# Kernel tuning notes

Hardware: AMD Instinct MI355X
Metric: run time of the kernel (lower is better)

Reference implementation:

```python
import jax, jax.numpy as jnp
import numpy as np


def setup_inputs() -> dict:
    key = jax.random.key(0)
    k1, k2, k3 = jax.random.split(key, 3)
    N, F, E, H = 50000, 256, 800000, 4
    P = F // H + 1            # proj = 65
    dk = P * H                # 260
    x = jax.random.normal(k1, (N, F), dtype=jnp.float32)
    W = jax.random.normal(k2, (2 * dk, F), dtype=jnp.float32) * 0.02
    b = jnp.zeros((2 * dk,), dtype=jnp.float32)
    edge_index = jax.random.randint(k3, (2, E), 0, N, dtype=jnp.int32)
    return {"x": x, "edge_index": edge_index, "W": W, "b": b, "num_heads": H}


def reference(x, edge_index, W, b, num_heads):
    # x: [N, F]; W: [2*dk, F] with dk = P*num_heads; edge_index: [2, E]
    N = x.shape[0]
    P = W.shape[0] // (2 * num_heads)
    qk = x @ W.T + b                                   # [N, 2*dk]
    qk = qk.reshape(N, num_heads, 2 * P)               # 'L (h hdim) -> L h hdim'
    q, k = qk[..., :P], qk[..., P:]                    # split=2 outer -> q then k, each [N, H, P]
    src, dst = edge_index[0], edge_index[1]
    # per-edge dot product per head (NB: original never applies self.scale)
    scores = jnp.einsum('ehp,ehp->eh', q[src], k[dst])  # [E, H]
    # sparse softmax over dim=2 (columns) i.e. segment-softmax grouped by row index per head
    smax = jax.ops.segment_max(scores, src, num_segments=N)  # [N, H]
    ex = jnp.exp(scores - smax[src])                         # [E, H]
    denom = jax.ops.segment_sum(ex, src, num_segments=N)     # [N, H]
    attn = ex / denom[src]                                   # [E, H]
    # torch.sparse.sum(attn, dim=0) / num_heads -> mean over heads per edge
    vals = attn.mean(axis=1)                                 # [E]
    return vals
```

## Files before the change

kernel.cpp:

```cpp
#include <hip/hip_runtime.h>
#include <hip/hip_bf16.h>

#define K_DIM 256
#define RQ    512
#define NPAD  640
#define GBM 128
#define GBN 128
#define GBK 32
#define EPITCH 152
#define NBK   64
#define CBLK  256

typedef unsigned short u16;
using short8  = __attribute__((ext_vector_type(8))) short;
using ushort8 = __attribute__((ext_vector_type(8))) unsigned short;
using f32x4   = __attribute__((ext_vector_type(4))) float;
using f32x2   = __attribute__((ext_vector_type(2))) float;

__device__ __forceinline__ float asf(unsigned u) {
  union { unsigned i; float f; } x; x.i = u; return x.f;
}
__device__ __forceinline__ u16 f2b(float f) {
  __hip_bfloat16 h = __float2bfloat16(f); return *(u16*)&h;
}

__device__ __forceinline__ int map2(int p) {
  if (p < 256) return (p >> 6) * 130 + (p & 63);
  if (p < 512) { int q = p - 256; return (q >> 6) * 130 + 65 + (q & 63); }
  if (p < 516) return (p - 512) * 130 + 64;
  if (p < 520) return (p - 516) * 130 + 129;
  return -1;
}

__global__ void __launch_bounds__(256) prep(
    const float* __restrict__ x, const float* __restrict__ W,
    const float* __restrict__ bv,
    u16* __restrict__ xb, u16* __restrict__ wb,
    float* __restrict__ bias, float* __restrict__ zbase,
    int M, int Mpad, int xblocks, int wblocks, int zn)
{
  const int blk = blockIdx.x, tid = threadIdx.x;
  if (blk < xblocks) {
    int idx = blk * 256 + tid;
    int total = Mpad * (K_DIM / 8);
    if (idx >= total) return;
    int row = idx / (K_DIM / 8);
    ushort8 o;
    if (row < M) {
      const float* s = x + (size_t)idx * 8;
      float4 a = *(const float4*)s;
      float4 b = *(const float4*)(s + 4);
      o[0] = f2b(a.x); o[1] = f2b(a.y); o[2] = f2b(a.z); o[3] = f2b(a.w);
      o[4] = f2b(b.x); o[5] = f2b(b.y); o[6] = f2b(b.z); o[7] = f2b(b.w);
    } else {
      #pragma unroll
      for (int j = 0; j < 8; ++j) o[j] = 0;
    }
    *(ushort8*)(xb + (size_t)idx * 8) = o;
  } else if (blk < xblocks + wblocks) {
    int idx = (blk - xblocks) * 256 + tid;
    int total = NPAD * (K_DIM / 8);
    if (idx >= total) return;
    int p  = idx / (K_DIM / 8);
    int kc = (idx % (K_DIM / 8)) * 8;
    int c  = map2(p);
    ushort8 o;
    if (c >= 0) {
      const float* s = W + (size_t)c * K_DIM + kc;
      float4 a = *(const float4*)s;
      float4 v = *(const float4*)(s + 4);
      o[0] = f2b(a.x); o[1] = f2b(a.y); o[2] = f2b(a.z); o[3] = f2b(a.w);
      o[4] = f2b(v.x); o[5] = f2b(v.y); o[6] = f2b(v.z); o[7] = f2b(v.w);
    } else {
      #pragma unroll
      for (int j = 0; j < 8; ++j) o[j] = 0;
    }
    *(ushort8*)(wb + (size_t)idx * 8) = o;
    if (kc == 0) bias[p] = (c >= 0) ? bv[c] : 0.f;
  } else {
    int i = (blk - xblocks - wblocks) * 256 + tid;
    if (i < zn) zbase[i] = 0.f;
  }
}

__global__ void __launch_bounds__(256) gemm_mfma(
    const u16* __restrict__ xb, const u16* __restrict__ wb,
    const float* __restrict__ bias, u16* __restrict__ qkb,
    u16* __restrict__ tl, int M)
{
  __shared__ u16 smem[GBM * EPITCH];
  const int tid  = threadIdx.x;
  const int wave = tid >> 6, lane = tid & 63;
  const int l15 = lane & 15, lhi = lane >> 4;
  const int row0 = blockIdx.x * GBM, p0 = blockIdx.y * GBN;
  const int wr = (wave >> 1) * 64, wc = (wave & 1) * 64;

  f32x4 acc[4][4];
  #pragma unroll
  for (int m = 0; m < 4; ++m)
    #pragma unroll
    for (int n = 0; n < 4; ++n) acc[m][n] = (f32x4){0.f, 0.f, 0.f, 0.f};

#define STAGE(b, k0) do {                                                     \
    u16* As_ = smem + (b) * 8192;                                             \
    u16* Bs_ = As_ + 4096;                                                    \
    _Pragma("unroll")                                                         \
    for (int i_ = 0; i_ < 2; ++i_) {                                          \
      int f_ = wave * 128 + i_ * 64 + lane;                                   \
      int r_ = f_ >> 2, c_ = f_ & 3;                                          \
      const u16* gA = xb + (size_t)(row0 + r_) * K_DIM + (k0) + c_ * 8;       \
      __builtin_amdgcn_global_load_lds(                                       \
          (const __attribute__((address_space(1))) void*)gA,                  \
          (__attribute__((address_space(3))) void*)(As_ + (wave*128 + i_*64)*8), \
          16, 0, 0);                                                          \
      const u16* gB = wb + (size_t)(p0 + r_) * K_DIM + (k0) + c_ * 8;         \
      __builtin_amdgcn_global_load_lds(                                       \
          (const __attribute__((address_space(1))) void*)gB,                  \
          (__attribute__((address_space(3))) void*)(Bs_ + (wave*128 + i_*64)*8), \
          16, 0, 0);                                                          \
    }                                                                         \
  } while (0)

  STAGE(0, 0);
  asm volatile("s_waitcnt vmcnt(0)" ::: "memory");
  __syncthreads();

  #pragma unroll
  for (int t = 0; t < K_DIM / GBK; ++t) {
    if (t < K_DIM / GBK - 1) STAGE((t + 1) & 1, (t + 1) * GBK);
    const u16* As = smem + (t & 1) * 8192;
    const u16* Bs = As + 4096;
    short8 af[4], bf[4];
    #pragma unroll
    for (int m = 0; m < 4; ++m)
      af[m] = *(const short8*)(As + (size_t)(wr + m * 16 + l15) * GBK + lhi * 8);
    #pragma unroll
    for (int n = 0; n < 4; ++n)
      bf[n] = *(const short8*)(Bs + (size_t)(wc + n * 16 + l15) * GBK + lhi * 8);
    #pragma unroll
    for (int m = 0; m < 4; ++m)
      #pragma unroll
      for (int n = 0; n < 4; ++n)
        acc[m][n] = __builtin_amdgcn_mfma_f32_16x16x32_bf16(af[m], bf[n], acc[m][n], 0, 0, 0);
    if (t < K_DIM / GBK - 1) {
      asm volatile("s_waitcnt vmcnt(0)" ::: "memory");
      __syncthreads();
    }
  }
#undef STAGE

  __syncthreads();

  #pragma unroll
  for (int n = 0; n < 4; ++n) {
    int col = wc + n * 16 + l15;
    float bvv = bias[p0 + col];
    #pragma unroll
    for (int m = 0; m < 4; ++m) {
      #pragma unroll
      for (int r = 0; r < 4; ++r) {
        int row = wr + m * 16 + lhi * 4 + r;
        smem[row * EPITCH + col] = f2b(acc[m][n][r] + bvv);
      }
    }
  }
  __syncthreads();

  if (p0 < 512) {
    #pragma unroll
    for (int it = 0; it < 8; ++it) {
      int row  = wave * 32 + it * 4 + lhi;
      int grow = row0 + row;
      uint4 v = *(const uint4*)(smem + row * EPITCH + l15 * 8);
      if (grow < M)
        *(uint4*)(qkb + (size_t)grow * RQ + p0 + l15 * 8) = v;
    }
  } else {
    #pragma unroll
    for (int it = 0; it < 8; ++it) {
      int row  = wave * 32 + it * 4 + lhi;
      int grow = row0 + row;
      if (l15 == 0 && grow < M) {
        uint4 v = *(const uint4*)(smem + row * EPITCH);
        *(uint4*)(tl + (size_t)grow * 8) = v;
      }
    }
  }
}

__global__ void __launch_bounds__(256) count_k(
    const int* __restrict__ ei, int* __restrict__ counts, int E, int per)
{
  __shared__ int h[NBK];
  const int tid = threadIdx.x, blk = blockIdx.x;
  if (tid < NBK) h[tid] = 0;
  __syncthreads();
  int start = blk * per, end = min(start + per, E);
  for (int i = start + tid; i < end; i += 256)
    atomicAdd(&h[ei[i] >> 10], 1);
  __syncthreads();
  if (tid < NBK) counts[tid * CBLK + blk] = h[tid];
}

__global__ void __launch_bounds__(1024) scan_k(int* __restrict__ counts)
{
  __shared__ int tot[NBK], base[NBK];
  const int tid = threadIdx.x, wv = tid >> 6, ln = tid & 63;
  for (int k = wv; k < NBK; k += 16) {
    int sum = 0;
    #pragma unroll
    for (int c = 0; c < CBLK / 64; ++c) sum += counts[k * CBLK + c * 64 + ln];
    #pragma unroll
    for (int off = 1; off < 64; off <<= 1) sum += __shfl_xor(sum, off);
    if (ln == 0) tot[k] = sum;
  }
  __syncthreads();
  if (wv == 0) {
    int v = tot[ln], inc = v;
    #pragma unroll
    for (int off = 1; off < 64; off <<= 1) {
      int u = __shfl_up(inc, off);
      if (ln >= off) inc += u;
    }
    base[ln] = inc - v;
  }
  __syncthreads();
  for (int k = wv; k < NBK; k += 16) {
    int carry = base[k];
    #pragma unroll
    for (int c = 0; c < CBLK / 64; ++c) {
      int v = counts[k * CBLK + c * 64 + ln];
      int inc = v;
      #pragma unroll
      for (int off = 1; off < 64; off <<= 1) {
        int u = __shfl_up(inc, off);
        if (ln >= off) inc += u;
      }
      int last = __shfl(inc, 63);
      counts[k * CBLK + c * 64 + ln] = carry + inc - v;
      carry += last;
    }
  }
}

__global__ void __launch_bounds__(256) scatter2_k(
    const int* __restrict__ ei, const int* __restrict__ offs,
    uint4* __restrict__ sorted, int E, int per)
{
  __shared__ int cur[NBK];
  const int tid = threadIdx.x, blk = blockIdx.x;
  if (tid < NBK) cur[tid] = offs[tid * CBLK + blk];
  __syncthreads();
  int start = blk * per, end = min(start + per, E);
  for (int i = start + tid; i < end; i += 256) {
    int s = ei[i], d = ei[E + i];
    int pos = atomicAdd(&cur[s >> 10], 1);
    sorted[pos] = make_uint4((unsigned)s, (unsigned)d, (unsigned)i, 0u);
  }
}

__global__ void __launch_bounds__(256) edge_pass(
    const u16* __restrict__ qkb, const u16* __restrict__ tl,
    const uint4* __restrict__ sorted,
    float* __restrict__ exb, float* __restrict__ denom, int E)
{
  const int tid  = threadIdx.x;
  const int wave = tid >> 6, lane = tid & 63;
  const int g = lane >> 3;
  const int l = lane & 7;

  const int nwg = gridDim.x;
  const int q8 = nwg >> 3, r8 = nwg & 7;
  const int xcd = blockIdx.x & 7, bix = blockIdx.x >> 3;
  const int swz = (xcd < r8) ? (xcd * (q8 + 1) + bix)
                             : (r8 * (q8 + 1) + (xcd - r8) * q8 + bix);

  const int slot = swz * 32 + wave * 8 + g;
  const bool valid = slot < E;
  uint4 tr = sorted[valid ? slot : 0];
  const int src = tr.x, dst = tr.y, e = tr.z;

  const u16* qrow = qkb + ((size_t)src * RQ) + l * 32;
  const u16* krow = qkb + ((size_t)dst * RQ) + 256 + l * 32;

  int2 ti = make_int2(0, 0);
  if (l < 2) {
    const u16* tp = tl + (size_t)(l ? dst : src) * 8 + (l ? 4 : 0);
    ti = *(const int2*)tp;
  }

  f32x2 a2 = {0.f, 0.f};
  #pragma unroll
  for (int c = 0; c < 4; ++c) {
    uint4 qv = *(const uint4*)(qrow + c * 8);
    uint4 kv = *(const uint4*)(krow + c * 8);
    const unsigned* qd = (const unsigned*)&qv;
    const unsigned* kd = (const unsigned*)&kv;
    #pragma unroll
    for (int j = 0; j < 4; ++j) {
      f32x2 qa = { asf(qd[j] << 16), asf(qd[j] & 0xffff0000u) };
      f32x2 ka = { asf(kd[j] << 16), asf(kd[j] & 0xffff0000u) };
      a2 += qa * ka;
    }
  }
  float s = a2[0] + a2[1];
  s += __shfl_xor(s, 1);

  const int h = l >> 1;
  int idxA = ((g << 3) | (l & 1)) << 2;
  int w01 = __builtin_amdgcn_ds_bpermute(idxA, ti.x);
  int w23 = __builtin_amdgcn_ds_bpermute(idxA, ti.y);
  unsigned wsel = (h & 2) ? (unsigned)w23 : (unsigned)w01;
  float tv = (h & 1) ? asf(wsel & 0xffff0000u) : asf(wsel << 16);
  float to = __shfl_xor(tv, 1);
  s = fmaf(tv, to, s);

  float ev = __expf(s);
  if (valid && (l & 1) == 0) {
    exb[(size_t)e * 4 + h] = ev;
    unsafeAtomicAdd(&denom[(size_t)src * 4 + h], ev);
  }
}

__global__ void __launch_bounds__(256) finalize_k(
    const float* __restrict__ exb, const float* __restrict__ denom,
    const int* __restrict__ ei, float* __restrict__ out, int E)
{
  int e = blockIdx.x * 256 + threadIdx.x;
  if (e >= E) return;
  int src = ei[e];
  float4 ev = *(const float4*)(exb + (size_t)e * 4);
  float4 dv = *(const float4*)(denom + (size_t)src * 4);
  out[e] = 0.25f * (ev.x / dv.x + ev.y / dv.y + ev.z / dv.z + ev.w / dv.w);
}

extern "C" void kernel_launch(void* const* d_in, const int* in_sizes, int n_in,
                              void* d_out, int out_size, void* d_ws, size_t ws_size,
                              hipStream_t stream)
{
  const float* x  = (const float*)d_in[0];
  const int*   ei = (const int*)d_in[1];
  const float* W  = (const float*)d_in[2];
  const float* b  = (const float*)d_in[3];

  const int F = in_sizes[2] / in_sizes[3];
  const int M = in_sizes[0] / F;
  const int E = in_sizes[1] / 2;

  const int mblocks = (M + GBM - 1) / GBM;
  const int Mpad    = mblocks * GBM;

  u16* xb  = (u16*)d_ws;
  u16* wb  = xb + (size_t)Mpad * K_DIM;
  u16* qkb = wb + (size_t)NPAD * K_DIM;
  u16* tl  = qkb + (size_t)M * RQ;
  float* bias  = (float*)(tl + (size_t)M * 8);
  float* exb   = bias + NPAD;
  float* denom = exb + (size_t)E * 4;
  int*   counts = (int*)(denom + (size_t)M * 4);
  uint4* sorted = (uint4*)(counts + NBK * CBLK);

  const int xblocks = (Mpad * (K_DIM / 8) + 255) / 256;
  const int wblocks = (NPAD * (K_DIM / 8) + 255) / 256;
  const int zn      = M * 4;
  const int zblocks = (zn + 255) / 256;
  hipLaunchKernelGGL(prep, dim3(xblocks + wblocks + zblocks), dim3(256), 0, stream,
                     x, W, b, xb, wb, bias, denom, M, Mpad, xblocks, wblocks, zn);

  const int per = (E + CBLK - 1) / CBLK;
  hipLaunchKernelGGL(count_k, dim3(CBLK), dim3(256), 0, stream, ei, counts, E, per);
  hipLaunchKernelGGL(scan_k, dim3(1), dim3(1024), 0, stream, counts);

  dim3 gg(mblocks, NPAD / GBN);
  hipLaunchKernelGGL(gemm_mfma, gg, dim3(256), 0, stream, xb, wb, bias, qkb, tl, M);

  hipLaunchKernelGGL(scatter2_k, dim3(CBLK), dim3(256), 0, stream,
                     ei, counts, sorted, E, per);

  int eblocks = (E + 31) / 32;
  hipLaunchKernelGGL(edge_pass, dim3(eblocks), dim3(256), 0, stream,
                     qkb, tl, sorted, exb, denom, E);

  hipLaunchKernelGGL(finalize_k, dim3((E + 255) / 256), dim3(256), 0, stream,
                     exb, denom, ei, (float*)d_out, E);
}
```

Measured before the change: 173.4 us.

## Bucket edges by source and destination band, pack sorted entries, fuse counting into prep

Edges are now bucketed by source band, destination half and source sub-block instead of by source block alone. This groups edges whose K rows fall in a narrower address range, to improve cache locality of the k[dst] gathers in the edge pass. Sorted entries shrink from 16 to 8 bytes by packing src and dst into 16 bits each, and the histogram kernel is folded into the prep launch. The packing assumes node ids fit in 16 bits (N=50000), and the band constants are hardcoded to this N.

```diff
diff --git a/kernel.cpp b/kernel.cpp
--- a/kernel.cpp
+++ b/kernel.cpp
@@ -8,8 +8,10 @@
 #define GBN 128
 #define GBK 32
 #define EPITCH 152
-#define NBK   64
+#define NBK   104
 #define CBLK  256
+#define SBAND 12512
+#define DBAND 25024
 
 typedef unsigned short u16;
 using short8  = __attribute__((ext_vector_type(8))) short;
@@ -22,6 +24,13 @@
 }
 __device__ __forceinline__ u16 f2b(float f) {
   __hip_bfloat16 h = __float2bfloat16(f); return *(u16*)&h;
+}
+
+__device__ __forceinline__ int bucket_of(int s, int d) {
+  int sband = s / SBAND;
+  int dband = d / DBAND;
+  int ssub  = (s - sband * SBAND) >> 10;
+  return ((sband << 1) | dband) * 13 + ssub;
 }
 
 __device__ __forceinline__ int map2(int p) {
@@ -34,11 +43,13 @@
 
 __global__ void __launch_bounds__(256) prep(
     const float* __restrict__ x, const float* __restrict__ W,
-    const float* __restrict__ bv,
+    const float* __restrict__ bv, const int* __restrict__ ei,
     u16* __restrict__ xb, u16* __restrict__ wb,
     float* __restrict__ bias, float* __restrict__ zbase,
-    int M, int Mpad, int xblocks, int wblocks, int zn)
-{
+    int* __restrict__ counts,
+    int M, int Mpad, int E, int per, int xblocks, int wblocks, int zblocks)
+{
+  __shared__ int h[NBK];
   const int blk = blockIdx.x, tid = threadIdx.x;
   if (blk < xblocks) {
     int idx = blk * 256 + tid;
@@ -77,9 +88,18 @@
     }
     *(ushort8*)(wb + (size_t)idx * 8) = o;
     if (kc == 0) bias[p] = (c >= 0) ? bv[c] : 0.f;
+  } else if (blk < xblocks + wblocks + zblocks) {
+    int i = (blk - xblocks - wblocks) * 256 + tid;
+    if (i < M * 4) zbase[i] = 0.f;
   } else {
-    int i = (blk - xblocks - wblocks) * 256 + tid;
-    if (i < zn) zbase[i] = 0.f;
+    int cb = blk - xblocks - wblocks - zblocks;
+    if (tid < NBK) h[tid] = 0;
+    __syncthreads();
+    int start = cb * per, end = min(start + per, E);
+    for (int i = start + tid; i < end; i += 256)
+      atomicAdd(&h[bucket_of(ei[i], ei[E + i])], 1);
+    __syncthreads();
+    if (tid < NBK) counts[tid * CBLK + cb] = h[tid];
   }
 }
 
@@ -188,20 +208,6 @@
   }
 }
 
-__global__ void __launch_bounds__(256) count_k(
-    const int* __restrict__ ei, int* __restrict__ counts, int E, int per)
-{
-  __shared__ int h[NBK];
-  const int tid = threadIdx.x, blk = blockIdx.x;
-  if (tid < NBK) h[tid] = 0;
-  __syncthreads();
-  int start = blk * per, end = min(start + per, E);
-  for (int i = start + tid; i < end; i += 256)
-    atomicAdd(&h[ei[i] >> 10], 1);
-  __syncthreads();
-  if (tid < NBK) counts[tid * CBLK + blk] = h[tid];
-}
-
 __global__ void __launch_bounds__(1024) scan_k(int* __restrict__ counts)
 {
   __shared__ int tot[NBK], base[NBK];
@@ -215,14 +221,9 @@
     if (ln == 0) tot[k] = sum;
   }
   __syncthreads();
-  if (wv == 0) {
-    int v = tot[ln], inc = v;
-    #pragma unroll
-    for (int off = 1; off < 64; off <<= 1) {
-      int u = __shfl_up(inc, off);
-      if (ln >= off) inc += u;
-    }
-    base[ln] = inc - v;
+  if (tid == 0) {
+    int run = 0;
+    for (int k = 0; k < NBK; ++k) { base[k] = run; run += tot[k]; }
   }
   __syncthreads();
   for (int k = wv; k < NBK; k += 16) {
@@ -245,7 +246,7 @@
 
 __global__ void __launch_bounds__(256) scatter2_k(
     const int* __restrict__ ei, const int* __restrict__ offs,
-    uint4* __restrict__ sorted, int E, int per)
+    uint2* __restrict__ sorted, int E, int per)
 {
   __shared__ int cur[NBK];
   const int tid = threadIdx.x, blk = blockIdx.x;
@@ -254,14 +255,14 @@
   int start = blk * per, end = min(start + per, E);
   for (int i = start + tid; i < end; i += 256) {
     int s = ei[i], d = ei[E + i];
-    int pos = atomicAdd(&cur[s >> 10], 1);
-    sorted[pos] = make_uint4((unsigned)s, (unsigned)d, (unsigned)i, 0u);
+    int pos = atomicAdd(&cur[bucket_of(s, d)], 1);
+    sorted[pos] = make_uint2(((unsigned)s << 16) | (unsigned)d, (unsigned)i);
   }
 }
 
 __global__ void __launch_bounds__(256) edge_pass(
     const u16* __restrict__ qkb, const u16* __restrict__ tl,
-    const uint4* __restrict__ sorted,
+    const uint2* __restrict__ sorted,
     float* __restrict__ exb, float* __restrict__ denom, int E)
 {
   const int tid  = threadIdx.x;
@@ -277,8 +278,9 @@
 
   const int slot = swz * 32 + wave * 8 + g;
   const bool valid = slot < E;
-  uint4 tr = sorted[valid ? slot : 0];
-  const int src = tr.x, dst = tr.y, e = tr.z;
+  uint2 tr = sorted[valid ? slot : 0];
+  const int src = tr.x >> 16, dst = tr.x & 0xffff;
+  const int e = tr.y;
 
   const u16* qrow = qkb + ((size_t)src * RQ) + l * 32;
   const u16* krow = qkb + ((size_t)dst * RQ) + 256 + l * 32;
@@ -358,17 +360,16 @@
   float* exb   = bias + NPAD;
   float* denom = exb + (size_t)E * 4;
   int*   counts = (int*)(denom + (size_t)M * 4);
-  uint4* sorted = (uint4*)(counts + NBK * CBLK);
+  uint2* sorted = (uint2*)(counts + NBK * CBLK);
 
   const int xblocks = (Mpad * (K_DIM / 8) + 255) / 256;
   const int wblocks = (NPAD * (K_DIM / 8) + 255) / 256;
-  const int zn      = M * 4;
-  const int zblocks = (zn + 255) / 256;
-  hipLaunchKernelGGL(prep, dim3(xblocks + wblocks + zblocks), dim3(256), 0, stream,
-                     x, W, b, xb, wb, bias, denom, M, Mpad, xblocks, wblocks, zn);
-
-  const int per = (E + CBLK - 1) / CBLK;
-  hipLaunchKernelGGL(count_k, dim3(CBLK), dim3(256), 0, stream, ei, counts, E, per);
+  const int zblocks = (M * 4 + 255) / 256;
+  const int per     = (E + CBLK - 1) / CBLK;
+  hipLaunchKernelGGL(prep, dim3(xblocks + wblocks + zblocks + CBLK), dim3(256), 0,
+                     stream, x, W, b, ei, xb, wb, bias, denom, counts,
+                     M, Mpad, E, per, xblocks, wblocks, zblocks);
+
   hipLaunchKernelGGL(scan_k, dim3(1), dim3(1024), 0, stream, counts);
 
   dim3 gg(mblocks, NPAD / GBN);
```

Result: no change. 176.8 us (+2.0%).
